# Performance work log

Measured on AMD Instinct MI355X. Metric: run time of the kernel, lower is better.

The kernel has to match this reference:

```python
import jax, jax.numpy as jnp
import numpy as np
from jax import lax

H, W, K, MAXN = 93, 44, 2, 24          # face grid, hop count, (2K+1)^2-1 neighbors
HID, LAT, OUT, B = 128, 1024, 2, 8


def _neighbor_lookup():
    """Static k-hop box neighbor indices/counts for each grid position."""
    HW = H * W
    idx = np.zeros((HW, MAXN), np.int32)
    cnt = np.zeros((HW,), np.int32)
    for r in range(H):
        for c in range(W):
            p = r * W + c
            n = []
            for dr in range(-K, K + 1):
                for dc in range(-K, K + 1):
                    if dr == 0 and dc == 0:
                        continue
                    rr, cc = r + dr, c + dc
                    if 0 <= rr < H and 0 <= cc < W:
                        n.append(rr * W + cc)
            cnt[p] = len(n)
            idx[p, :len(n)] = n
    return jnp.asarray(idx), jnp.asarray(cnt)


def _gelu(x):
    return jax.nn.gelu(x, approximate=False)  # torch default GELU is exact erf


def _group_norm(x, gamma, beta, groups=8, eps=1e-5):
    b, c, h, w = x.shape
    xg = x.reshape(b, groups, c // groups, h, w)
    mu = xg.mean(axis=(2, 3, 4), keepdims=True)
    var = xg.var(axis=(2, 3, 4), keepdims=True)
    xg = (xg - mu) * lax.rsqrt(var + eps)
    return xg.reshape(b, c, h, w) * gamma[None, :, None, None] + beta[None, :, None, None]


def setup_inputs() -> dict:
    key = jax.random.key(0)
    ks = jax.random.split(key, 10)
    s = 0.05
    nbr_idx, nbr_cnt = _neighbor_lookup()
    return {
        "face_tensor": jax.random.normal(ks[0], (B, 2, H, W), jnp.float32),
        "latent_token": jax.random.normal(ks[1], (B, LAT), jnp.float32),
        "mask_2d": jax.random.randint(ks[2], (B, H, W), 0, 2, jnp.int32),
        "nbr_indices": nbr_idx,
        "nbr_counts": nbr_cnt,
        # latent_proj
        "Wl": jax.random.normal(ks[3], (LAT, HID), jnp.float32) * s,
        "bl": jnp.zeros((HID,), jnp.float32),
        # global_decoder: ConvTranspose2d(3x3,pad1) -> GN(8) -> GELU -> Conv2d(3x3,pad1) -> GELU
        "Wt": jax.random.normal(ks[4], (3, 3, HID, HID), jnp.float32) * s,
        "bt": jnp.zeros((HID,), jnp.float32),
        "g1": jnp.ones((HID,), jnp.float32),
        "b1g": jnp.zeros((HID,), jnp.float32),
        "Wc": jax.random.normal(ks[5], (3, 3, HID, HID), jnp.float32) * s,
        "bc": jnp.zeros((HID,), jnp.float32),
        # attention scorer
        "Wa": jax.random.normal(ks[6], (HID,), jnp.float32) * s,
        "ba": jnp.zeros((), jnp.float32),
        # masked_pred_head MLP
        "W1": jax.random.normal(ks[7], (2 * HID, HID), jnp.float32) * s,
        "b1": jnp.zeros((HID,), jnp.float32),
        "W2": jax.random.normal(ks[8], (HID, OUT), jnp.float32) * s,
        "b2": jnp.zeros((OUT,), jnp.float32),
    }


def reference(face_tensor, latent_token, mask_2d, nbr_indices, nbr_counts,
              Wl, bl, Wt, bt, g1, b1g, Wc, bc, Wa, ba, W1, b1, W2, b2):
    Bn, C, Hh, Ww = face_tensor.shape
    HW = Hh * Ww
    dn = ("NCHW", "HWIO", "NCHW")

    # --- feature extraction (global decoder branch) ---
    latent_cond = _gelu(latent_token @ Wl + bl)                      # (B, HID)
    x = jnp.broadcast_to(latent_cond[:, :, None, None], (Bn, HID, Hh, Ww))
    f = lax.conv_transpose(x, Wt, (1, 1), "SAME", dimension_numbers=dn) + bt[None, :, None, None]
    f = _gelu(_group_norm(f, g1, b1g))
    f = lax.conv_general_dilated(f, Wc, (1, 1), "SAME", dimension_numbers=dn) + bc[None, :, None, None]
    f = _gelu(f)
    feats = f.reshape(Bn, HID, HW).transpose(0, 2, 1)                # (B, HW, HID)

    # --- masked-neighbor attention pooling (computed for every position, padded layout) ---
    mask_flat = mask_2d.reshape(Bn, HW)
    in_range = jnp.arange(MAXN)[None, :] < nbr_counts[:, None]        # (HW, 24)
    nbr_masked = jnp.take(mask_flat, nbr_indices, axis=1)             # (B, HW, 24)
    valid = in_range[None] & (nbr_masked == 0)
    nbr_feat = jnp.take(feats, nbr_indices, axis=1)                   # (B, HW, 24, HID)
    logits = jnp.einsum("bpnh,h->bpn", nbr_feat, Wa) + ba
    logits = jnp.where(valid, logits, jnp.float32(-10000.0))
    attn = jax.nn.softmax(logits, axis=-1)
    attended = jnp.einsum("bpn,bpnh->bph", attn, nbr_feat)            # (B, HW, HID)

    combined = jnp.concatenate(
        [attended, jnp.broadcast_to(latent_cond[:, None, :], (Bn, HW, HID))], axis=-1)
    preds = _gelu(combined @ W1 + b1) @ W2 + b2                       # (B, HW, OUT)

    # --- pack masked positions to front of each row (fixed capacity HW instead of dynamic max_masked) ---
    m = mask_flat > 0
    within = jnp.cumsum(m, axis=1) - 1                                # slot for each masked position
    tgt = jnp.where(m, within, HW)                                    # unmasked go to dump slot HW
    brow = jnp.arange(Bn)[:, None]
    pred_packed = jnp.zeros((Bn, HW + 1, OUT), preds.dtype).at[brow, tgt].set(preds)[:, :HW]
    pos = jnp.arange(HW)
    rc = jnp.stack([pos // Ww, pos % Ww], axis=-1).astype(jnp.int32)  # (HW, 2)
    mask_indices = jnp.zeros((Bn, HW + 1, 2), jnp.int32).at[brow, tgt].set(
        jnp.broadcast_to(rc[None], (Bn, HW, 2)))[:, :HW]
    valid_mask = jnp.zeros((Bn, HW + 1), bool).at[brow, tgt].set(m)[:, :HW]
    return pred_packed, mask_indices, valid_mask
```

## Files before the change

kernel.cpp:

```cpp
#include <hip/hip_runtime.h>
#include <cmath>

#define HH   93
#define WWID 44
#define HWSZ 4092
#define NMAX 24
#define HID  128
#define LATD 1024
#define NB   8

__device__ __forceinline__ float gelu_f(float x) {
  return 0.5f * x * (1.0f + erff(x * 0.70710678118654752440f));
}

__device__ __constant__ int c_map[5][3] = {{-1,0,1},{0,1,1},{1,1,1},{1,1,2},{1,2,-1}};

__global__ __launch_bounds__(256) void k_tap(
    const float* __restrict__ latent, const float* __restrict__ Wl,
    const float* __restrict__ bl,
    const float* __restrict__ Wt, const float* __restrict__ W1, const float* __restrict__ b1p,
    float* __restrict__ u, float* __restrict__ cbo, float* __restrict__ outz)
{
  const int tap = blockIdx.x, b = blockIdx.y, tid = threadIdx.x;
  const int h4 = tid & 31, ig = tid >> 5;
  __shared__ float lc_s[HID];
  __shared__ float red[8 * HID];

  {
    const int gtid = (b * 10 + tap) * 256 + tid;
    float4* oz = (float4*)outz;
    const float4 z = make_float4(0.f, 0.f, 0.f, 0.f);
    for (int i = gtid; i < (NB*HWSZ*5)/4; i += 20480) oz[i] = z;
  }

  {
    const float* lat = latent + b * LATD;
    const float4* w4 = (const float4*)Wl;
    float4 a = make_float4(0.f, 0.f, 0.f, 0.f);
    #pragma unroll 8
    for (int i = 0; i < 128; ++i) {
      const int L = ig * 128 + i;
      const float lv = lat[L];
      const float4 wv = w4[L*32 + h4];
      a.x = fmaf(lv, wv.x, a.x); a.y = fmaf(lv, wv.y, a.y);
      a.z = fmaf(lv, wv.z, a.z); a.w = fmaf(lv, wv.w, a.w);
    }
    ((float4*)red)[ig*32 + h4] = a;
  }
  __syncthreads();
  if (tid < HID) {
    float s = bl[tid];
    #pragma unroll
    for (int g = 0; g < 8; ++g) s += red[g*HID + tid];
    lc_s[tid] = gelu_f(s);
  }
  __syncthreads();

  const float4* w4 = (tap < 9) ? ((const float4*)(Wt + tap*HID*HID))
                               : ((const float4*)(W1 + HID*HID));
  float4 a = make_float4(0.f, 0.f, 0.f, 0.f);
  #pragma unroll
  for (int i = 0; i < 16; ++i) {
    const int I = ig*16 + i;
    const float lv = lc_s[I];
    const float4 wv = w4[I*32 + h4];
    a.x = fmaf(lv, wv.x, a.x); a.y = fmaf(lv, wv.y, a.y);
    a.z = fmaf(lv, wv.z, a.z); a.w = fmaf(lv, wv.w, a.w);
  }
  __syncthreads();
  ((float4*)red)[ig*32 + h4] = a;
  __syncthreads();
  if (tid < HID) {
    float s = 0.f;
    #pragma unroll
    for (int g = 0; g < 8; ++g) s += red[g*HID + tid];
    if (tap < 9) u[(b*10 + tap)*HID + tid] = s;
    else         cbo[b*HID + tid] = b1p[tid] + s;
  }
}

__global__ __launch_bounds__(256) void k_pre2(
    const float* __restrict__ u, const float* __restrict__ bt,
    const float* __restrict__ g1p, const float* __restrict__ b1g,
    const float* __restrict__ Wc, float* __restrict__ t2o)
{
  const int tap = blockIdx.x, b = blockIdx.y, tid = threadIdx.x;
  const int o4 = tid & 31, ig = tid >> 5;
  __shared__ float f2s[9 * HID];
  __shared__ float red[8 * 9 * HID];
  if (tid < HID) {
    const int t = tid;
    float uv[9];
    #pragma unroll
    for (int k = 0; k < 9; ++k) uv[k] = u[(b*10 + k)*HID + t];
    float ur[3][3];
    #pragma unroll
    for (int kc = 0; kc < 3; ++kc) {
      ur[0][kc] = uv[3+kc] + uv[6+kc];
      ur[1][kc] = uv[0+kc] + uv[3+kc] + uv[6+kc];
      ur[2][kc] = uv[0+kc] + uv[3+kc];
    }
    const float btv = bt[t];
    float f1v[9];
    #pragma unroll
    for (int a = 0; a < 3; ++a) {
      f1v[a*3+0] = btv + ur[a][1] + ur[a][2];
      f1v[a*3+1] = btv + ur[a][0] + ur[a][1] + ur[a][2];
      f1v[a*3+2] = btv + ur[a][0] + ur[a][1];
    }
    const float wr[3] = {1.f, (float)(HH-2), 1.f};
    const float wc[3] = {1.f, (float)(WWID-2), 1.f};
    float s1 = 0.f, s2 = 0.f;
    #pragma unroll
    for (int a = 0; a < 3; ++a)
      #pragma unroll
      for (int c = 0; c < 3; ++c) {
        const float w = wr[a] * wc[c];
        const float v = f1v[a*3+c];
        s1 += w * v;
        s2 += w * v * v;
      }
    #pragma unroll
    for (int off = 1; off < 16; off <<= 1) {
      s1 += __shfl_xor(s1, off);
      s2 += __shfl_xor(s2, off);
    }
    const float invN = 1.f / (float)(16 * HWSZ);
    const float mean = s1 * invN;
    const float var  = s2 * invN - mean * mean;
    const float sc = rsqrtf(var + 1e-5f) * g1p[t];
    const float sh = b1g[t] - mean * sc;
    #pragma unroll
    for (int k = 0; k < 9; ++k)
      f2s[k*HID + t] = gelu_f(fmaf(f1v[k], sc, sh));
  }
  __syncthreads();
  const float4* w4 = (const float4*)(Wc + tap*HID*HID);
  float4 acc[9];
  #pragma unroll
  for (int k = 0; k < 9; ++k) acc[k] = make_float4(0.f, 0.f, 0.f, 0.f);
  #pragma unroll
  for (int i = 0; i < 16; ++i) {
    const int I = ig*16 + i;
    const float4 wv = w4[I*32 + o4];
    #pragma unroll
    for (int k = 0; k < 9; ++k) {
      const float f = f2s[k*HID + I];
      acc[k].x = fmaf(f, wv.x, acc[k].x);
      acc[k].y = fmaf(f, wv.y, acc[k].y);
      acc[k].z = fmaf(f, wv.z, acc[k].z);
      acc[k].w = fmaf(f, wv.w, acc[k].w);
    }
  }
  #pragma unroll
  for (int k = 0; k < 9; ++k)
    ((float4*)red)[(ig*9 + k)*32 + o4] = acc[k];
  __syncthreads();
  for (int j = tid; j < 9*HID; j += 256) {
    float s = 0.f;
    #pragma unroll
    for (int g = 0; g < 8; ++g) s += red[g*9*HID + j];
    t2o[(b*9 + tap)*9*HID + j] = s;
  }
}

__global__ __launch_bounds__(256) void k_pre3(
    const float* __restrict__ t2i, const float* __restrict__ bc,
    const float* __restrict__ Wa, const float* __restrict__ ba,
    const float* __restrict__ W1,
    float* __restrict__ logito, float* __restrict__ projo)
{
  const int bid = blockIdx.x, b = bid / 25, cs = bid % 25;
  const int r5 = cs / 5, c5 = cs % 5, tid = threadIdx.x;
  __shared__ float f3s[HID];
  __shared__ float red2[2];
  __shared__ float redp[8 * HID];
  if (tid < HID) {
    float acc = bc[tid];
    #pragma unroll
    for (int kr = 0; kr < 3; ++kr) {
      const int rm = c_map[r5][kr];
      if (rm < 0) continue;
      #pragma unroll
      for (int kc = 0; kc < 3; ++kc) {
        const int cm = c_map[c5][kc];
        if (cm < 0) continue;
        acc += t2i[((b*9 + kr*3 + kc)*9 + rm*3 + cm)*HID + tid];
      }
    }
    const float f3v = gelu_f(acc);
    f3s[tid] = f3v;
    float pl = f3v * Wa[tid];
    #pragma unroll
    for (int off = 1; off < 64; off <<= 1) pl += __shfl_xor(pl, off);
    if ((tid & 63) == 0) red2[tid >> 6] = pl;
  }
  __syncthreads();
  const int h4 = tid & 31, og = tid >> 5;
  const float4* w4 = (const float4*)W1;
  float4 a = make_float4(0.f, 0.f, 0.f, 0.f);
  #pragma unroll
  for (int i = 0; i < 16; ++i) {
    const int o = og*16 + i;
    const float f = f3s[o];
    const float4 wv = w4[o*32 + h4];
    a.x = fmaf(f, wv.x, a.x); a.y = fmaf(f, wv.y, a.y);
    a.z = fmaf(f, wv.z, a.z); a.w = fmaf(f, wv.w, a.w);
  }
  ((float4*)redp)[og*32 + h4] = a;
  __syncthreads();
  if (tid < HID) {
    float s = 0.f;
    #pragma unroll
    for (int g = 0; g < 8; ++g) s += redp[g*HID + tid];
    projo[(b*25 + cs)*HID + tid] = s;
  }
  if (tid == 0) logito[b*32 + cs] = red2[0] + red2[1] + ba[0];
}

__global__ __launch_bounds__(256) void k_pospack(
    const int* __restrict__ mask, const int* __restrict__ nbr_idx, const int* __restrict__ nbr_cnt,
    const int* __restrict__ , const float* __restrict__ logiti,
    const float* __restrict__ proji, const float* __restrict__ cbasei,
    const float* __restrict__ W2, const float* __restrict__ b2,
    float* __restrict__ out)
{
  const int b = blockIdx.y, chunk = blockIdx.x, tid = threadIdx.x;
  __shared__ float4 proj_s[25 * 32];
  __shared__ float4 cbase_s[32];
  __shared__ float  logit_s[32];
  __shared__ float  w2_s[2 * HID];
  __shared__ float  ippart[2][2];
  __shared__ int    bcnt_s[4];
  __shared__ int    wcnt_s[4];

  const float4* pj = (const float4*)(proji + b*25*HID);
  for (int i = tid; i < 25*32; i += 256) proj_s[i] = pj[i];
  if (tid < 32) cbase_s[tid] = ((const float4*)(cbasei + b*HID))[tid];
  if (tid < 32) logit_s[tid] = (tid < 25) ? logiti[b*32 + tid] : 0.f;
  w2_s[tid] = W2[tid];

  const int p0 = chunk * 128;
  {
    int cnt = 0;
    const int4* m4 = (const int4*)(mask + b*HWSZ);
    for (int i = tid; i < (p0 >> 2); i += 256) {
      const int4 v = m4[i];
      cnt += (v.x > 0) + (v.y > 0) + (v.z > 0) + (v.w > 0);
    }
    #pragma unroll
    for (int off = 1; off < 64; off <<= 1) cnt += __shfl_xor(cnt, off);
    if ((tid & 63) == 0) bcnt_s[tid >> 6] = cnt;
  }
  __syncthreads();

  if (tid < HID) {
    const float g = gelu_f(((const float*)proj_s)[12*HID + tid] + ((const float*)cbase_s)[tid]);
    float q0 = g * w2_s[tid*2 + 0];
    float q1 = g * w2_s[tid*2 + 1];
    #pragma unroll
    for (int off = 1; off < 64; off <<= 1) {
      q0 += __shfl_xor(q0, off);
      q1 += __shfl_xor(q1, off);
    }
    if ((tid & 63) == 0) { ippart[tid >> 6][0] = q0; ippart[tid >> 6][1] = q1; }
  }
  __syncthreads();
  const int   base = bcnt_s[0] + bcnt_s[1] + bcnt_s[2] + bcnt_s[3];
  const float ip0 = ippart[0][0] + ippart[1][0] + b2[0];
  const float ip1 = ippart[0][1] + ippart[1][1] + b2[1];

  const int p = p0 + (tid >> 1);
  const int half = tid & 1;
  const bool pok = (p < HWSZ);
  const int pc = pok ? p : 0;
  const int r = pc / WWID, cc = pc % WWID;
  const bool interior = (r >= 4) && (r <= HH-5) && (cc >= 4) && (cc <= WWID-5);
  const bool mp = pok && (mask[b*HWSZ + pc] > 0);

  float pr0 = ip0, pr1 = ip1;
  if (pok && !interior) {
    const int cnt = nbr_cnt[pc];
    float ev[NMAX];
    int   cid[NMAX];
    #pragma unroll
    for (int n = 0; n < NMAX; ++n) {
      const int q = nbr_idx[pc*NMAX + n];
      const int qr = q / WWID, qc = q % WWID;
      const int r5 = (qr == 0) ? 0 : (qr == 1) ? 1 : (qr == HH-2) ? 3 : (qr == HH-1) ? 4 : 2;
      const int c5 = (qc == 0) ? 0 : (qc == 1) ? 1 : (qc == WWID-2) ? 3 : (qc == WWID-1) ? 4 : 2;
      const int cd = r5*5 + c5;
      cid[n] = cd;
      const bool ok = (n < cnt) && (mask[b*HWSZ + q] == 0);
      ev[n] = ok ? logit_s[cd] : -10000.0f;
    }
    float mx = ev[0];
    #pragma unroll
    for (int n = 1; n < NMAX; ++n) mx = fmaxf(mx, ev[n]);
    float s = 0.f;
    #pragma unroll
    for (int n = 0; n < NMAX; ++n) { ev[n] = expf(ev[n] - mx); s += ev[n]; }
    const float inv = 1.f / s;

    float a0 = 0.f, a1 = 0.f;
    const int hb = half * 16;
    #pragma unroll 4
    for (int hq = 0; hq < 16; ++hq) {
      float4 a = make_float4(0.f, 0.f, 0.f, 0.f);
      #pragma unroll
      for (int n = 0; n < NMAX; ++n) {
        const float4 pv = proj_s[cid[n]*32 + hb + hq];
        const float w = ev[n];
        a.x = fmaf(w, pv.x, a.x);
        a.y = fmaf(w, pv.y, a.y);
        a.z = fmaf(w, pv.z, a.z);
        a.w = fmaf(w, pv.w, a.w);
      }
      const float4 cb = cbase_s[hb + hq];
      const int h0 = (hb + hq) * 4;
      const float g0 = gelu_f(fmaf(inv, a.x, cb.x));
      const float g1v = gelu_f(fmaf(inv, a.y, cb.y));
      const float g2 = gelu_f(fmaf(inv, a.z, cb.z));
      const float g3 = gelu_f(fmaf(inv, a.w, cb.w));
      a0 = fmaf(g0, w2_s[(h0+0)*2+0], a0); a1 = fmaf(g0, w2_s[(h0+0)*2+1], a1);
      a0 = fmaf(g1v, w2_s[(h0+1)*2+0], a0); a1 = fmaf(g1v, w2_s[(h0+1)*2+1], a1);
      a0 = fmaf(g2, w2_s[(h0+2)*2+0], a0); a1 = fmaf(g2, w2_s[(h0+2)*2+1], a1);
      a0 = fmaf(g3, w2_s[(h0+3)*2+0], a0); a1 = fmaf(g3, w2_s[(h0+3)*2+1], a1);
    }
    a0 += __shfl_xor(a0, 1);
    a1 += __shfl_xor(a1, 1);
    pr0 = a0 + b2[0];
    pr1 = a1 + b2[1];
  }

  const unsigned long long bal = __ballot(mp && half == 0);
  const int lane = tid & 63;
  const int myidx = __popcll(bal & ((1ull << lane) - 1ull));
  if (lane == 0) wcnt_s[tid >> 6] = (int)__popcll(bal);
  __syncthreads();
  int wbase = 0;
  for (int w = 0; w < (tid >> 6); ++w) wbase += wcnt_s[w];
  if (mp && half == 0) {
    const int slot = base + wbase + myidx;
    float* predo = out + b*HWSZ*2;
    float* idxo  = out + NB*HWSZ*2 + b*HWSZ*2;
    float* valo  = out + NB*HWSZ*4 + b*HWSZ;
    predo[slot*2 + 0] = pr0;
    predo[slot*2 + 1] = pr1;
    idxo[slot*2 + 0] = (float)r;
    idxo[slot*2 + 1] = (float)cc;
    valo[slot] = 1.0f;
  }
}

extern "C" void kernel_launch(void* const* d_in, const int* in_sizes, int n_in,
                              void* d_out, int out_size, void* d_ws, size_t ws_size,
                              hipStream_t stream) {
  (void)in_sizes; (void)n_in; (void)out_size; (void)ws_size;
  const float* latent  = (const float*)d_in[1];
  const int*   mask    = (const int*)d_in[2];
  const int*   nbr_idx = (const int*)d_in[3];
  const int*   nbr_cnt = (const int*)d_in[4];
  const float* Wl  = (const float*)d_in[5];
  const float* bl  = (const float*)d_in[6];
  const float* Wt  = (const float*)d_in[7];
  const float* bt  = (const float*)d_in[8];
  const float* g1p = (const float*)d_in[9];
  const float* b1g = (const float*)d_in[10];
  const float* Wc  = (const float*)d_in[11];
  const float* bc  = (const float*)d_in[12];
  const float* Wa  = (const float*)d_in[13];
  const float* ba  = (const float*)d_in[14];
  const float* W1  = (const float*)d_in[15];
  const float* b1p = (const float*)d_in[16];
  const float* W2  = (const float*)d_in[17];
  const float* b2  = (const float*)d_in[18];

  float* ws    = (float*)d_ws;
  float* u     = ws;
  float* t2    = ws + 10240;
  float* logit = ws + 93184;
  float* proj  = ws + 93440;
  float* cbase = ws + 119040;

  dim3 gA(10, NB);
  k_tap<<<gA, 256, 0, stream>>>(latent, Wl, bl, Wt, W1, b1p, u, cbase, (float*)d_out);
  dim3 gB(9, NB);
  k_pre2<<<gB, 256, 0, stream>>>(u, bt, g1p, b1g, Wc, t2);
  k_pre3<<<NB*25, 256, 0, stream>>>(t2, bc, Wa, ba, W1, logit, proj);
  dim3 gC(32, NB);
  k_pospack<<<gC, 256, 0, stream>>>(mask, nbr_idx, nbr_cnt, nullptr, logit, proj, cbase, W2, b2,
                                    (float*)d_out);
}
```

Measured before the change: 56.61 us.

## Split latent projection into separate split-K kernel instead of recomputing per tap block

Moves the latent-to-hidden projection out of k_tap, where each of the 10 tap blocks per batch recomputed the full 1024-length reduction, into a new kernel that splits the reduction across 16 blocks per batch and writes partial sums. k_tap now sums the 16 partials before applying GELU. Output zeroing also moves to the new kernel. This removes redundant serial work and raises parallelism, at the price of an extra kernel launch and a workspace round trip.

```diff
diff --git a/kernel.cpp b/kernel.cpp
--- a/kernel.cpp
+++ b/kernel.cpp
@@ -15,47 +15,59 @@
 
 __device__ __constant__ int c_map[5][3] = {{-1,0,1},{0,1,1},{1,1,1},{1,1,2},{1,2,-1}};
 
+__global__ __launch_bounds__(256) void k_lc_part(
+    const float* __restrict__ latent, const float* __restrict__ Wl,
+    float* __restrict__ part, float* __restrict__ outz)
+{
+  const int split = blockIdx.x, b = blockIdx.y, tid = threadIdx.x;
+  const int h4 = tid & 31, ig = tid >> 5;
+
+  {
+    const int gtid = (b * 16 + split) * 256 + tid;
+    float4* oz = (float4*)outz;
+    const float4 z = make_float4(0.f, 0.f, 0.f, 0.f);
+    for (int i = gtid; i < (NB*HWSZ*5)/4; i += 32768) oz[i] = z;
+  }
+
+  const int L0 = split * 64 + ig * 8;
+  const float* lat = latent + b * LATD;
+  const float4* w4 = (const float4*)Wl;
+  float4 a = make_float4(0.f, 0.f, 0.f, 0.f);
+  #pragma unroll
+  for (int i = 0; i < 8; ++i) {
+    const int L = L0 + i;
+    const float lv = lat[L];
+    const float4 wv = w4[L*32 + h4];
+    a.x = fmaf(lv, wv.x, a.x); a.y = fmaf(lv, wv.y, a.y);
+    a.z = fmaf(lv, wv.z, a.z); a.w = fmaf(lv, wv.w, a.w);
+  }
+  __shared__ float red[8 * HID];
+  ((float4*)red)[ig*32 + h4] = a;
+  __syncthreads();
+  if (tid < HID) {
+    float s = 0.f;
+    #pragma unroll
+    for (int g = 0; g < 8; ++g) s += red[g*HID + tid];
+    part[(b*16 + split)*HID + tid] = s;
+  }
+}
+
 __global__ __launch_bounds__(256) void k_tap(
-    const float* __restrict__ latent, const float* __restrict__ Wl,
-    const float* __restrict__ bl,
+    const float* __restrict__ part, const float* __restrict__ bl,
     const float* __restrict__ Wt, const float* __restrict__ W1, const float* __restrict__ b1p,
-    float* __restrict__ u, float* __restrict__ cbo, float* __restrict__ outz)
+    float* __restrict__ u, float* __restrict__ cbo)
 {
   const int tap = blockIdx.x, b = blockIdx.y, tid = threadIdx.x;
   const int h4 = tid & 31, ig = tid >> 5;
   __shared__ float lc_s[HID];
   __shared__ float red[8 * HID];
-
-  {
-    const int gtid = (b * 10 + tap) * 256 + tid;
-    float4* oz = (float4*)outz;
-    const float4 z = make_float4(0.f, 0.f, 0.f, 0.f);
-    for (int i = gtid; i < (NB*HWSZ*5)/4; i += 20480) oz[i] = z;
-  }
-
-  {
-    const float* lat = latent + b * LATD;
-    const float4* w4 = (const float4*)Wl;
-    float4 a = make_float4(0.f, 0.f, 0.f, 0.f);
-    #pragma unroll 8
-    for (int i = 0; i < 128; ++i) {
-      const int L = ig * 128 + i;
-      const float lv = lat[L];
-      const float4 wv = w4[L*32 + h4];
-      a.x = fmaf(lv, wv.x, a.x); a.y = fmaf(lv, wv.y, a.y);
-      a.z = fmaf(lv, wv.z, a.z); a.w = fmaf(lv, wv.w, a.w);
-    }
-    ((float4*)red)[ig*32 + h4] = a;
-  }
-  __syncthreads();
   if (tid < HID) {
     float s = bl[tid];
     #pragma unroll
-    for (int g = 0; g < 8; ++g) s += red[g*HID + tid];
+    for (int sp = 0; sp < 16; ++sp) s += part[(b*16 + sp)*HID + tid];
     lc_s[tid] = gelu_f(s);
   }
   __syncthreads();
-
   const float4* w4 = (tap < 9) ? ((const float4*)(Wt + tap*HID*HID))
                                : ((const float4*)(W1 + HID*HID));
   float4 a = make_float4(0.f, 0.f, 0.f, 0.f);
@@ -67,7 +79,6 @@
     a.x = fmaf(lv, wv.x, a.x); a.y = fmaf(lv, wv.y, a.y);
     a.z = fmaf(lv, wv.z, a.z); a.w = fmaf(lv, wv.w, a.w);
   }
-  __syncthreads();
   ((float4*)red)[ig*32 + h4] = a;
   __syncthreads();
   if (tid < HID) {
@@ -220,7 +231,7 @@
 
 __global__ __launch_bounds__(256) void k_pospack(
     const int* __restrict__ mask, const int* __restrict__ nbr_idx, const int* __restrict__ nbr_cnt,
-    const int* __restrict__ , const float* __restrict__ logiti,
+    const float* __restrict__ logiti,
     const float* __restrict__ proji, const float* __restrict__ cbasei,
     const float* __restrict__ W2, const float* __restrict__ b2,
     float* __restrict__ out)
@@ -382,13 +393,16 @@
   float* logit = ws + 93184;
   float* proj  = ws + 93440;
   float* cbase = ws + 119040;
-
+  float* part  = ws + 120064;
+
+  dim3 g0(16, NB);
+  k_lc_part<<<g0, 256, 0, stream>>>(latent, Wl, part, (float*)d_out);
   dim3 gA(10, NB);
-  k_tap<<<gA, 256, 0, stream>>>(latent, Wl, bl, Wt, W1, b1p, u, cbase, (float*)d_out);
+  k_tap<<<gA, 256, 0, stream>>>(part, bl, Wt, W1, b1p, u, cbase);
   dim3 gB(9, NB);
   k_pre2<<<gB, 256, 0, stream>>>(u, bt, g1p, b1g, Wc, t2);
   k_pre3<<<NB*25, 256, 0, stream>>>(t2, bc, Wa, ba, W1, logit, proj);
   dim3 gC(32, NB);
-  k_pospack<<<gC, 256, 0, stream>>>(mask, nbr_idx, nbr_cnt, nullptr, logit, proj, cbase, W2, b2,
+  k_pospack<<<gC, 256, 0, stream>>>(mask, nbr_idx, nbr_cnt, logit, proj, cbase, W2, b2,
                                     (float*)d_out);
 }
```

New measurement: 48.07 us. 15.1% less time.

## Fuse conv and case-projection kernels, widen latent-projection kernel to 1024 threads

Applied to the files above, without the earlier changes.

Merges the second conv stage (k_pre2) and the per-case attention/projection stage (k_pre3) into one kernel, k_case, launched with one block per (case, batch). Each block recomputes the group-norm/GELU features and accumulates only the conv taps its boundary case needs, so the 9x9 intermediate workspace round-trip and one launch go away. The first kernel now uses 1024 threads per block, which splits the latent reduction four times wider and zeroes the output with a single store per thread instead of a strided loop. In exchange the normalization is recomputed in every block and Wc reads are repeated across cases.

```diff
diff --git a/kernel.cpp b/kernel.cpp
--- a/kernel.cpp
+++ b/kernel.cpp
@@ -15,7 +15,7 @@
 
 __device__ __constant__ int c_map[5][3] = {{-1,0,1},{0,1,1},{1,1,1},{1,1,2},{1,2,-1}};
 
-__global__ __launch_bounds__(256) void k_tap(
+__global__ __launch_bounds__(1024) void k_tap10(
     const float* __restrict__ latent, const float* __restrict__ Wl,
     const float* __restrict__ bl,
     const float* __restrict__ Wt, const float* __restrict__ W1, const float* __restrict__ b1p,
@@ -23,71 +23,86 @@
 {
   const int tap = blockIdx.x, b = blockIdx.y, tid = threadIdx.x;
   const int h4 = tid & 31, ig = tid >> 5;
+  __shared__ float red[32 * HID];
   __shared__ float lc_s[HID];
-  __shared__ float red[8 * HID];
 
   {
-    const int gtid = (b * 10 + tap) * 256 + tid;
+    const int gtid = (b * 10 + tap) * 1024 + tid;
     float4* oz = (float4*)outz;
-    const float4 z = make_float4(0.f, 0.f, 0.f, 0.f);
-    for (int i = gtid; i < (NB*HWSZ*5)/4; i += 20480) oz[i] = z;
+    if (gtid < (NB*HWSZ*5)/4) oz[gtid] = make_float4(0.f, 0.f, 0.f, 0.f);
   }
 
   {
     const float* lat = latent + b * LATD;
     const float4* w4 = (const float4*)Wl;
     float4 a = make_float4(0.f, 0.f, 0.f, 0.f);
+    for (int i0 = 0; i0 < 32; i0 += 8) {
+      float  lv[8];
+      float4 wv[8];
+      #pragma unroll
+      for (int j = 0; j < 8; ++j) {
+        const int L = ig*32 + i0 + j;
+        lv[j] = lat[L];
+        wv[j] = w4[L*32 + h4];
+      }
+      #pragma unroll
+      for (int j = 0; j < 8; ++j) {
+        a.x = fmaf(lv[j], wv[j].x, a.x);
+        a.y = fmaf(lv[j], wv[j].y, a.y);
+        a.z = fmaf(lv[j], wv[j].z, a.z);
+        a.w = fmaf(lv[j], wv[j].w, a.w);
+      }
+    }
+    ((float4*)red)[ig*32 + h4] = a;
+  }
+  __syncthreads();
+  if (tid < HID) {
+    float s = bl[tid];
     #pragma unroll 8
-    for (int i = 0; i < 128; ++i) {
-      const int L = ig * 128 + i;
-      const float lv = lat[L];
-      const float4 wv = w4[L*32 + h4];
-      a.x = fmaf(lv, wv.x, a.x); a.y = fmaf(lv, wv.y, a.y);
-      a.z = fmaf(lv, wv.z, a.z); a.w = fmaf(lv, wv.w, a.w);
-    }
-    ((float4*)red)[ig*32 + h4] = a;
-  }
-  __syncthreads();
-  if (tid < HID) {
-    float s = bl[tid];
-    #pragma unroll
-    for (int g = 0; g < 8; ++g) s += red[g*HID + tid];
+    for (int g = 0; g < 32; ++g) s += red[g*HID + tid];
     lc_s[tid] = gelu_f(s);
   }
   __syncthreads();
 
-  const float4* w4 = (tap < 9) ? ((const float4*)(Wt + tap*HID*HID))
-                               : ((const float4*)(W1 + HID*HID));
-  float4 a = make_float4(0.f, 0.f, 0.f, 0.f);
+  const float4* wt4 = (tap < 9) ? ((const float4*)(Wt + tap*HID*HID))
+                                : ((const float4*)(W1 + HID*HID));
+  float4 aa = make_float4(0.f, 0.f, 0.f, 0.f);
   #pragma unroll
-  for (int i = 0; i < 16; ++i) {
-    const int I = ig*16 + i;
+  for (int j = 0; j < 4; ++j) {
+    const int I = ig*4 + j;
     const float lv = lc_s[I];
-    const float4 wv = w4[I*32 + h4];
-    a.x = fmaf(lv, wv.x, a.x); a.y = fmaf(lv, wv.y, a.y);
-    a.z = fmaf(lv, wv.z, a.z); a.w = fmaf(lv, wv.w, a.w);
-  }
-  __syncthreads();
-  ((float4*)red)[ig*32 + h4] = a;
+    const float4 wv = wt4[I*32 + h4];
+    aa.x = fmaf(lv, wv.x, aa.x); aa.y = fmaf(lv, wv.y, aa.y);
+    aa.z = fmaf(lv, wv.z, aa.z); aa.w = fmaf(lv, wv.w, aa.w);
+  }
+  __syncthreads();
+  ((float4*)red)[ig*32 + h4] = aa;
   __syncthreads();
   if (tid < HID) {
     float s = 0.f;
-    #pragma unroll
-    for (int g = 0; g < 8; ++g) s += red[g*HID + tid];
+    #pragma unroll 8
+    for (int g = 0; g < 32; ++g) s += red[g*HID + tid];
     if (tap < 9) u[(b*10 + tap)*HID + tid] = s;
     else         cbo[b*HID + tid] = b1p[tid] + s;
   }
 }
 
-__global__ __launch_bounds__(256) void k_pre2(
+__global__ __launch_bounds__(256) void k_case(
     const float* __restrict__ u, const float* __restrict__ bt,
     const float* __restrict__ g1p, const float* __restrict__ b1g,
-    const float* __restrict__ Wc, float* __restrict__ t2o)
+    const float* __restrict__ Wc, const float* __restrict__ bc,
+    const float* __restrict__ Wa, const float* __restrict__ ba,
+    const float* __restrict__ W1,
+    float* __restrict__ logito, float* __restrict__ projo)
 {
-  const int tap = blockIdx.x, b = blockIdx.y, tid = threadIdx.x;
-  const int o4 = tid & 31, ig = tid >> 5;
+  const int cs = blockIdx.x, b = blockIdx.y;
+  const int r5 = cs / 5, c5 = cs % 5;
+  const int tid = threadIdx.x, o4 = tid & 31, ig = tid >> 5;
   __shared__ float f2s[9 * HID];
-  __shared__ float red[8 * 9 * HID];
+  __shared__ float red[8 * HID];
+  __shared__ float f3s[HID];
+  __shared__ float red2[2];
+
   if (tid < HID) {
     const int t = tid;
     float uv[9];
@@ -135,84 +150,61 @@
       f2s[k*HID + t] = gelu_f(fmaf(f1v[k], sc, sh));
   }
   __syncthreads();
-  const float4* w4 = (const float4*)(Wc + tap*HID*HID);
-  float4 acc[9];
+
+  float4 a = make_float4(0.f, 0.f, 0.f, 0.f);
   #pragma unroll
-  for (int k = 0; k < 9; ++k) acc[k] = make_float4(0.f, 0.f, 0.f, 0.f);
+  for (int kr = 0; kr < 3; ++kr) {
+    const int rm = c_map[r5][kr];
+    if (rm < 0) continue;
+    #pragma unroll
+    for (int kc = 0; kc < 3; ++kc) {
+      const int cm = c_map[c5][kc];
+      if (cm < 0) continue;
+      const float4* w4 = (const float4*)(Wc + (kr*3 + kc)*HID*HID);
+      const float* f2p = &f2s[(rm*3 + cm)*HID];
+      #pragma unroll
+      for (int i = 0; i < 16; ++i) {
+        const int I = ig*16 + i;
+        const float f = f2p[I];
+        const float4 wv = w4[I*32 + o4];
+        a.x = fmaf(f, wv.x, a.x); a.y = fmaf(f, wv.y, a.y);
+        a.z = fmaf(f, wv.z, a.z); a.w = fmaf(f, wv.w, a.w);
+      }
+    }
+  }
+  ((float4*)red)[ig*32 + o4] = a;
+  __syncthreads();
+
+  if (tid < HID) {
+    float s = bc[tid];
+    #pragma unroll
+    for (int g = 0; g < 8; ++g) s += red[g*HID + tid];
+    const float f3v = gelu_f(s);
+    f3s[tid] = f3v;
+    float pl = f3v * Wa[tid];
+    #pragma unroll
+    for (int off = 1; off < 64; off <<= 1) pl += __shfl_xor(pl, off);
+    if ((tid & 63) == 0) red2[tid >> 6] = pl;
+  }
+  __syncthreads();
+
+  const float4* w14 = (const float4*)W1;
+  float4 aa = make_float4(0.f, 0.f, 0.f, 0.f);
   #pragma unroll
   for (int i = 0; i < 16; ++i) {
     const int I = ig*16 + i;
-    const float4 wv = w4[I*32 + o4];
-    #pragma unroll
-    for (int k = 0; k < 9; ++k) {
-      const float f = f2s[k*HID + I];
-      acc[k].x = fmaf(f, wv.x, acc[k].x);
-      acc[k].y = fmaf(f, wv.y, acc[k].y);
-      acc[k].z = fmaf(f, wv.z, acc[k].z);
-      acc[k].w = fmaf(f, wv.w, acc[k].w);
-    }
-  }
-  #pragma unroll
-  for (int k = 0; k < 9; ++k)
-    ((float4*)red)[(ig*9 + k)*32 + o4] = acc[k];
-  __syncthreads();
-  for (int j = tid; j < 9*HID; j += 256) {
+    const float f = f3s[I];
+    const float4 wv = w14[I*32 + o4];
+    aa.x = fmaf(f, wv.x, aa.x); aa.y = fmaf(f, wv.y, aa.y);
+    aa.z = fmaf(f, wv.z, aa.z); aa.w = fmaf(f, wv.w, aa.w);
+  }
+  __syncthreads();
+  ((float4*)red)[ig*32 + o4] = aa;
+  __syncthreads();
+  if (tid < HID) {
     float s = 0.f;
     #pragma unroll
-    for (int g = 0; g < 8; ++g) s += red[g*9*HID + j];
-    t2o[(b*9 + tap)*9*HID + j] = s;
-  }
-}
-
-__global__ __launch_bounds__(256) void k_pre3(
-    const float* __restrict__ t2i, const float* __restrict__ bc,
-    const float* __restrict__ Wa, const float* __restrict__ ba,
-    const float* __restrict__ W1,
-    float* __restrict__ logito, float* __restrict__ projo)
-{
-  const int bid = blockIdx.x, b = bid / 25, cs = bid % 25;
-  const int r5 = cs / 5, c5 = cs % 5, tid = threadIdx.x;
-  __shared__ float f3s[HID];
-  __shared__ float red2[2];
-  __shared__ float redp[8 * HID];
-  if (tid < HID) {
-    float acc = bc[tid];
-    #pragma unroll
-    for (int kr = 0; kr < 3; ++kr) {
-      const int rm = c_map[r5][kr];
-      if (rm < 0) continue;
-      #pragma unroll
-      for (int kc = 0; kc < 3; ++kc) {
-        const int cm = c_map[c5][kc];
-        if (cm < 0) continue;
-        acc += t2i[((b*9 + kr*3 + kc)*9 + rm*3 + cm)*HID + tid];
-      }
-    }
-    const float f3v = gelu_f(acc);
-    f3s[tid] = f3v;
-    float pl = f3v * Wa[tid];
-    #pragma unroll
-    for (int off = 1; off < 64; off <<= 1) pl += __shfl_xor(pl, off);
-    if ((tid & 63) == 0) red2[tid >> 6] = pl;
-  }
-  __syncthreads();
-  const int h4 = tid & 31, og = tid >> 5;
-  const float4* w4 = (const float4*)W1;
-  float4 a = make_float4(0.f, 0.f, 0.f, 0.f);
-  #pragma unroll
-  for (int i = 0; i < 16; ++i) {
-    const int o = og*16 + i;
-    const float f = f3s[o];
-    const float4 wv = w4[o*32 + h4];
-    a.x = fmaf(f, wv.x, a.x); a.y = fmaf(f, wv.y, a.y);
-    a.z = fmaf(f, wv.z, a.z); a.w = fmaf(f, wv.w, a.w);
-  }
-  ((float4*)redp)[og*32 + h4] = a;
-  __syncthreads();
-  if (tid < HID) {
-    float s = 0.f;
-    #pragma unroll
-    for (int g = 0; g < 8; ++g) s += redp[g*HID + tid];
+    for (int g = 0; g < 8; ++g) s += red[g*HID + tid];
     projo[(b*25 + cs)*HID + tid] = s;
   }
   if (tid == 0) logito[b*32 + cs] = red2[0] + red2[1] + ba[0];
@@ -220,7 +212,7 @@
 
 __global__ __launch_bounds__(256) void k_pospack(
     const int* __restrict__ mask, const int* __restrict__ nbr_idx, const int* __restrict__ nbr_cnt,
-    const int* __restrict__ , const float* __restrict__ logiti,
+    const float* __restrict__ logiti,
     const float* __restrict__ proji, const float* __restrict__ cbasei,
     const float* __restrict__ W2, const float* __restrict__ b2,
     float* __restrict__ out)
@@ -378,17 +370,15 @@
 
   float* ws    = (float*)d_ws;
   float* u     = ws;
-  float* t2    = ws + 10240;
-  float* logit = ws + 93184;
-  float* proj  = ws + 93440;
-  float* cbase = ws + 119040;
+  float* logit = ws + 10240;
+  float* proj  = ws + 10496;
+  float* cbase = ws + 36096;
 
   dim3 gA(10, NB);
-  k_tap<<<gA, 256, 0, stream>>>(latent, Wl, bl, Wt, W1, b1p, u, cbase, (float*)d_out);
-  dim3 gB(9, NB);
-  k_pre2<<<gB, 256, 0, stream>>>(u, bt, g1p, b1g, Wc, t2);
-  k_pre3<<<NB*25, 256, 0, stream>>>(t2, bc, Wa, ba, W1, logit, proj);
+  k_tap10<<<gA, 1024, 0, stream>>>(latent, Wl, bl, Wt, W1, b1p, u, cbase, (float*)d_out);
+  dim3 gB(25, NB);
+  k_case<<<gB, 256, 0, stream>>>(u, bt, g1p, b1g, Wc, bc, Wa, ba, W1, logit, proj);
   dim3 gC(32, NB);
-  k_pospack<<<gC, 256, 0, stream>>>(mask, nbr_idx, nbr_cnt, nullptr, logit, proj, cbase, W2, b2,
+  k_pospack<<<gC, 256, 0, stream>>>(mask, nbr_idx, nbr_cnt, logit, proj, cbase, W2, b2,
                                     (float*)d_out);
 }
```

New measurement: 47.07 us. 16.8% less time.
